# Optimization experiments

Hardware: AMD Instinct MI355X
Metric: run time of the kernel (lower is better)

Reference implementation:

```python
import jax, jax.numpy as jnp
import numpy as np

IN_CH = 256
OUT_CH = 256
NUM_HEADS = 4
LOCAL_RADIUS = 2
SCALE = OUT_CH ** 0.5  # torch divides by out_channels**0.5


def setup_inputs() -> dict:
    key = jax.random.key(0)
    ks = jax.random.split(key, 7)
    B, C, H, W = 1, IN_CH, 48, 48
    x = jax.random.normal(ks[0], (B, C, H, W), dtype=jnp.float32)
    s = 0.02
    Wq = jax.random.normal(ks[1], (OUT_CH, IN_CH), dtype=jnp.float32) * s
    Wk = jax.random.normal(ks[2], (OUT_CH, IN_CH), dtype=jnp.float32) * s
    Wv = jax.random.normal(ks[3], (OUT_CH, IN_CH), dtype=jnp.float32) * s
    bq = jax.random.normal(ks[4], (OUT_CH,), dtype=jnp.float32) * s
    bk = jax.random.normal(ks[5], (OUT_CH,), dtype=jnp.float32) * s
    bv = jax.random.normal(ks[6], (OUT_CH,), dtype=jnp.float32) * s
    return {"x": x, "Wq": Wq, "bq": bq, "Wk": Wk, "bk": bk, "Wv": Wv, "bv": bv}


def reference(x, Wq, bq, Wk, bk, Wv, bv):
    B, C, H, W = x.shape
    N = H * W
    # Faithful to torch: x.view(B, N, -1) is a raw reshape of [B,C,H,W]
    xr = x.reshape(B, N, C)
    q = xr @ Wq.T + bq  # [B, N, OUT_CH]
    k = xr @ Wk.T + bk
    v = xr @ Wv.T + bv
    dh = OUT_CH // NUM_HEADS
    # [B, heads, N, dh]
    q = q.reshape(B, N, NUM_HEADS, dh).transpose(0, 2, 1, 3)
    k = k.reshape(B, N, NUM_HEADS, dh).transpose(0, 2, 1, 3)
    v = v.reshape(B, N, NUM_HEADS, dh).transpose(0, 2, 1, 3)
    acc = jnp.zeros_like(v)
    for h in range(-LOCAL_RADIUS, LOCAL_RADIUS + 1):
        for w in range(-LOCAL_RADIUS, LOCAL_RADIUS + 1):
            # torch rolls dims (-3, -2) of [B, heads, N, dh] -> axes (1, 2)
            rk = jnp.roll(k, shift=(h, w), axis=(1, 2))
            scores = jnp.einsum('bhnd,bhmd->bhnm', q, rk) / SCALE
            p = jax.nn.softmax(scores, axis=-1)  # dropout p=0 -> identity
            rv = jnp.roll(v, shift=(-h, -w), axis=(1, 2))
            acc = acc + jnp.einsum('bhnm,bhmd->bhnd', p, rv)
    out = acc.transpose(0, 2, 1, 3).reshape(B, N, NUM_HEADS * dh)
    return out
```

## Files before the change

kernel.cpp:

```cpp
#include <hip/hip_runtime.h>


#define N_TOK 2304
#define OUTC 256
#define HSZ (N_TOK * 64)

typedef _Float16 half8 __attribute__((ext_vector_type(8)));
typedef _Float16 half4 __attribute__((ext_vector_type(4)));
typedef float f32x4 __attribute__((ext_vector_type(4)));

typedef __attribute__((address_space(3))) unsigned int as3_u32;
typedef __attribute__((address_space(1))) unsigned int as1_u32;

__device__ __forceinline__ f32x4 mfma16(half8 a, half8 b, f32x4 c) {
  return __builtin_amdgcn_mfma_f32_16x16x32_f16(a, b, c, 0, 0, 0);
}

__device__ __forceinline__ void gload_lds16(const _Float16* g, _Float16* l) {
  __builtin_amdgcn_global_load_lds((const as1_u32*)g, (as3_u32*)l, 16, 0, 0);
}

__global__ __launch_bounds__(256) void k_convert(
    const float* __restrict__ x, const float* __restrict__ Wq,
    const float* __restrict__ Wk, const float* __restrict__ Wv,
    _Float16* __restrict__ xh, _Float16* __restrict__ Wh) {
  int i = blockIdx.x * 256 + threadIdx.x;
  if (i < N_TOK * OUTC / 4) {
    float4 f = ((const float4*)x)[i];
    half4 h; h[0] = (_Float16)f.x; h[1] = (_Float16)f.y; h[2] = (_Float16)f.z; h[3] = (_Float16)f.w;
    ((half4*)xh)[i] = h;
  }
  if (i < OUTC * OUTC / 4) {
    float4 a = ((const float4*)Wq)[i];
    float4 b = ((const float4*)Wk)[i];
    float4 c = ((const float4*)Wv)[i];
    half4 ha, hb, hc;
    ha[0]=(_Float16)a.x; ha[1]=(_Float16)a.y; ha[2]=(_Float16)a.z; ha[3]=(_Float16)a.w;
    hb[0]=(_Float16)b.x; hb[1]=(_Float16)b.y; hb[2]=(_Float16)b.z; hb[3]=(_Float16)b.w;
    hc[0]=(_Float16)c.x; hc[1]=(_Float16)c.y; hc[2]=(_Float16)c.z; hc[3]=(_Float16)c.w;
    ((half4*)Wh)[i] = ha;
    ((half4*)(Wh + OUTC*OUTC))[i] = hb;
    ((half4*)(Wh + 2*OUTC*OUTC))[i] = hc;
  }
}

__global__ __launch_bounds__(256) void k_proj(
    const _Float16* __restrict__ xh, const _Float16* __restrict__ Wh,
    const float* __restrict__ bq, const float* __restrict__ bk,
    const float* __restrict__ bv,
    _Float16* __restrict__ Qh, _Float16* __restrict__ KF, float* __restrict__ VfT) {
  const int w = threadIdx.x >> 6, lane = threadIdx.x & 63;
  const int lr = lane & 15, lk = lane >> 4;
  const int n0 = blockIdx.x * 64 + w * 16;
  const int o0 = blockIdx.y * 64;
  const int mat = blockIdx.z;
  const _Float16* W = Wh + mat * (OUTC * OUTC);
  f32x4 acc[4] = {};
  const _Float16* xrow = xh + (n0 + lr) * OUTC + 8 * lk;
#pragma unroll
  for (int kk = 0; kk < 8; ++kk) {
    half8 a = *(const half8*)(xrow + 32 * kk);
#pragma unroll
    for (int c = 0; c < 4; ++c) {
      half8 b = *(const half8*)(W + (o0 + 16*c + lr) * OUTC + 32*kk + 8*lk);
      acc[c] = mfma16(a, b, acc[c]);
    }
  }
  const float* bias = (mat == 0) ? bq : (mat == 1) ? bk : bv;
  const int hd = blockIdx.y;
#pragma unroll
  for (int c = 0; c < 4; ++c) {
    int o = o0 + 16*c + lr;
    float bo = bias[o];
    if (mat == 2) {
      float4 vv;
      vv.x = acc[c][0] + bo; vv.y = acc[c][1] + bo;
      vv.z = acc[c][2] + bo; vv.w = acc[c][3] + bo;
      *(float4*)(VfT + (size_t)o * N_TOK + n0 + 4*lk) = vv;
    } else if (mat == 0) {
      int d = 16*c + lr;
      const float qs = 0.0625f * 1.4426950408889634f;
#pragma unroll
      for (int r = 0; r < 4; ++r) {
        int n = n0 + 4*lk + r;
        Qh[((size_t)hd * N_TOK + n) * 64 + d] = (_Float16)((acc[c][r] + bo) * qs);
      }
    } else {
      int d = 16*c + lr;
      int h = d >> 5, g4K = (d >> 3) & 3, iiK = d & 7;
#pragma unroll
      for (int r = 0; r < 4; ++r) {
        int n = n0 + 4*lk + r;
        int tK = n >> 6, cK = (n >> 4) & 3, lrK = n & 15;
        KF[(size_t)hd * HSZ + ((tK*4 + cK)*2 + h)*512 + (g4K*16 + lrK)*8 + iiK] =
            (_Float16)(acc[c][r] + bo);
      }
    }
  }
}

__global__ __launch_bounds__(256) void k_smooth(
    const float* __restrict__ VfT, _Float16* __restrict__ VF) {
  const int t = blockIdx.x, vh = blockIdx.y;
  for (int f = threadIdx.x; f < 512; f += 256) {
    int cc = f >> 7, h = (f >> 6) & 1, g4 = (f >> 4) & 3, lr = f & 15;
    const float* src = VfT + (size_t)(vh*64 + 16*cc + lr) * N_TOK;
    int jbase = t*64 + 32*h + 4*g4;
    half8 out;
#pragma unroll
    for (int i = 0; i < 8; ++i) {
      int j = jbase + 16*(i >> 2) + (i & 3);
      float s = 0.f;
#pragma unroll
      for (int w = -4; w <= 4; w += 2) s += src[(j + w + N_TOK) % N_TOK];
      out[i] = (_Float16)s;
    }
    *(half8*)(VF + (size_t)vh * HSZ + (size_t)t * 4096 + f * 8) = out;
  }
}

__global__ __launch_bounds__(256) void k_flash(
    const _Float16* __restrict__ Qh, const _Float16* __restrict__ KF,
    const _Float16* __restrict__ VF,
    _Float16* __restrict__ Opart, float* __restrict__ Lpart) {
  __shared__ __align__(16) _Float16 lds[2][8192];
  const int wv = threadIdx.x >> 6, lane = threadIdx.x & 63;
  const int lr = lane & 15, g4 = lane >> 4;
  const int strip = blockIdx.x * 4 + wv;
  const int n0 = strip * 16;
  const int pair = blockIdx.y;
  const int hd = pair >> 2, gk = pair & 3;
  const int chunk = blockIdx.z;
  const int vh = (2*hd + 4 - gk) & 3;

  const _Float16* Qp = Qh + ((size_t)hd * N_TOK + n0 + lr) * 64 + 8*g4;
  const half8 q0 = *(const half8*)(Qp);
  const half8 q1 = *(const half8*)(Qp + 32);

  const _Float16* Kt = KF + (size_t)gk * HSZ + (size_t)chunk * 9 * 4096;
  const _Float16* Vt = VF + (size_t)vh * HSZ + (size_t)chunk * 9 * 4096;
  const _Float16* gsrc = (wv < 2 ? Kt : Vt) + (wv & 1) * 2048 + lane * 8;
  const int ldsoff = (wv < 2 ? 0 : 4096) + (wv & 1) * 2048;

  f32x4 acc[4] = {};
  f32x4 accl = {};
  half8 ones;
#pragma unroll
  for (int i = 0; i < 8; ++i) ones[i] = (_Float16)1.0f;

  auto stage = [&](int t, int b) {
    const _Float16* s = gsrc + (size_t)t * 4096;
    _Float16* d = &lds[b][ldsoff];
    gload_lds16(s,        d);
    gload_lds16(s + 512,  d + 512);
    gload_lds16(s + 1024, d + 1024);
    gload_lds16(s + 1536, d + 1536);
  };
  auto body = [&](int b) {
    const _Float16* ldsK = &lds[b][0]    + lane * 8;
    const _Float16* ldsV = &lds[b][4096] + lane * 8;
    f32x4 s[4];
    __builtin_amdgcn_s_setprio(1);
#pragma unroll
    for (int c = 0; c < 4; ++c) {
      f32x4 t = {};
      t = mfma16(*(const half8*)(ldsK + c*1024),       q0, t);
      t = mfma16(*(const half8*)(ldsK + c*1024 + 512), q1, t);
      s[c] = t;
    }
    __builtin_amdgcn_s_setprio(0);
    float p[16];
#pragma unroll
    for (int c = 0; c < 4; ++c)
#pragma unroll
      for (int r = 0; r < 4; ++r) p[4*c + r] = exp2f(s[c][r]);
    half8 pb0, pb1;
#pragma unroll
    for (int ii = 0; ii < 8; ++ii) { pb0[ii] = (_Float16)p[ii]; pb1[ii] = (_Float16)p[8 + ii]; }
    __builtin_amdgcn_s_setprio(1);
#pragma unroll
    for (int cc = 0; cc < 4; ++cc) {
      acc[cc] = mfma16(*(const half8*)(ldsV + cc*1024),       pb0, acc[cc]);
      acc[cc] = mfma16(*(const half8*)(ldsV + cc*1024 + 512), pb1, acc[cc]);
    }
    accl = mfma16(ones, pb0, accl);
    accl = mfma16(ones, pb1, accl);
    __builtin_amdgcn_s_setprio(0);
  };

  stage(0, 0);
  __syncthreads();
#pragma unroll 1
  for (int t = 0; t < 9; ++t) {
    if (t < 8) stage(t + 1, (t + 1) & 1);
    body(t & 1);
    __syncthreads();
  }

  float inv = 1.0f / accl[0];
  _Float16* Od = Opart + (((size_t)chunk * 16 + pair) * N_TOK + n0 + lr) * 64;
#pragma unroll
  for (int cc = 0; cc < 4; ++cc) {
    half4 h;
#pragma unroll
    for (int r = 0; r < 4; ++r) h[r] = (_Float16)(acc[cc][r] * inv);
    *(half4*)(Od + 16*cc + 4*g4) = h;
  }
  if (g4 == 0)
    Lpart[((size_t)chunk * 16 + pair) * N_TOK + n0 + lr] = accl[0];
}

__global__ __launch_bounds__(256) void k_combine(
    const _Float16* __restrict__ Opart, const float* __restrict__ Lpart,
    float* __restrict__ out) {
  int gid = blockIdx.x * 256 + threadIdx.x;
  int hd = gid / (N_TOK * 8);
  int rem = gid % (N_TOK * 8);
  int n = rem >> 3, db = (rem & 7) * 8;
  float acc[8] = {};
#pragma unroll
  for (int gk = 0; gk < 4; ++gk) {
    float cg = (((hd - gk) & 3) == 2) ? 2.0f : 1.0f;
    int pair = hd * 4 + gk;
    float la[4], lsum = 0.f;
#pragma unroll
    for (int ch = 0; ch < 4; ++ch) {
      la[ch] = Lpart[((size_t)ch * 16 + pair) * N_TOK + n];
      lsum += la[ch];
    }
    float rs = cg / lsum;
#pragma unroll
    for (int ch = 0; ch < 4; ++ch) {
      half8 v = *(const half8*)(Opart + (((size_t)ch * 16 + pair) * N_TOK + n) * 64 + db);
      float w = la[ch] * rs;
#pragma unroll
      for (int i = 0; i < 8; ++i) acc[i] += w * (float)v[i];
    }
  }
  float* dst = out + (size_t)n * OUTC + hd * 64 + db;
  float4 r0, r1;
  r0.x = acc[0]; r0.y = acc[1]; r0.z = acc[2]; r0.w = acc[3];
  r1.x = acc[4]; r1.y = acc[5]; r1.z = acc[6]; r1.w = acc[7];
  *(float4*)(dst)     = r0;
  *(float4*)(dst + 4) = r1;
}

extern "C" void kernel_launch(void* const* d_in, const int* in_sizes, int n_in,
                              void* d_out, int out_size, void* d_ws, size_t ws_size,
                              hipStream_t stream) {
  (void)in_sizes; (void)n_in; (void)out_size; (void)ws_size;
  const float* x  = (const float*)d_in[0];
  const float* Wq = (const float*)d_in[1];
  const float* bq = (const float*)d_in[2];
  const float* Wk = (const float*)d_in[3];
  const float* bk = (const float*)d_in[4];
  const float* Wv = (const float*)d_in[5];
  const float* bv = (const float*)d_in[6];

  char* ws = (char*)d_ws;
  _Float16* xh  = (_Float16*)(ws);
  float*    Lp  = (float*)   (ws);
  _Float16* Wh  = (_Float16*)(ws + 1179648);
  _Float16* Qh  = (_Float16*)(ws + 1572864);
  _Float16* KF  = (_Float16*)(ws + 2752512);
  float*    VfT = (float*)   (ws + 3932160);
  _Float16* VF  = (_Float16*)(ws + 6291456);
  _Float16* Op  = (_Float16*)(ws + 7471104);
  float* out = (float*)d_out;

  k_convert<<<dim3(576), dim3(256), 0, stream>>>(x, Wq, Wk, Wv, xh, Wh);
  k_proj   <<<dim3(36, 4, 3), dim3(256), 0, stream>>>(xh, Wh, bq, bk, bv, Qh, KF, VfT);
  k_smooth <<<dim3(36, 4), dim3(256), 0, stream>>>(VfT, VF);
  k_flash  <<<dim3(36, 16, 4), dim3(256), 0, stream>>>(Qh, KF, VF, Op, Lp);
  k_combine<<<dim3(288), dim3(256), 0, stream>>>(Op, Lp, out);
}
```

Baseline: 73.97 us.

## Process two 16-row query strips per wave to reuse K/V tiles

Each wave now handles 32 query rows (two 16-row strips) instead of 16. It reuses every K and V fragment loaded from LDS for both strips, and the grid along x is halved. Each K/V chunk is therefore staged through LDS half as many times, which cuts global-to-LDS traffic and block overhead. The softmax exponent now uses the raw exp2 builtin with packed round-toward-zero fp16 conversion to trim ALU work. In exchange the kernel uses more registers and launches half as many blocks (1152 instead of 2304), which may lower occupancy and latency hiding.

```diff
diff --git a/kernel.cpp b/kernel.cpp
--- a/kernel.cpp
+++ b/kernel.cpp
@@ -7,6 +7,7 @@
 
 typedef _Float16 half8 __attribute__((ext_vector_type(8)));
 typedef _Float16 half4 __attribute__((ext_vector_type(4)));
+typedef __fp16 fp16x2 __attribute__((ext_vector_type(2)));
 typedef float f32x4 __attribute__((ext_vector_type(4)));
 
 typedef __attribute__((address_space(3))) unsigned int as3_u32;
@@ -19,6 +20,8 @@
 __device__ __forceinline__ void gload_lds16(const _Float16* g, _Float16* l) {
   __builtin_amdgcn_global_load_lds((const as1_u32*)g, (as3_u32*)l, 16, 0, 0);
 }
+
+union H8U { half8 h8; fp16x2 h2[4]; };
 
 __global__ __launch_bounds__(256) void k_convert(
     const float* __restrict__ x, const float* __restrict__ Wq,
@@ -127,23 +130,25 @@
   const int wv = threadIdx.x >> 6, lane = threadIdx.x & 63;
   const int lr = lane & 15, g4 = lane >> 4;
   const int strip = blockIdx.x * 4 + wv;
-  const int n0 = strip * 16;
+  const int n0 = strip * 32;
   const int pair = blockIdx.y;
   const int hd = pair >> 2, gk = pair & 3;
   const int chunk = blockIdx.z;
   const int vh = (2*hd + 4 - gk) & 3;
 
   const _Float16* Qp = Qh + ((size_t)hd * N_TOK + n0 + lr) * 64 + 8*g4;
-  const half8 q0 = *(const half8*)(Qp);
-  const half8 q1 = *(const half8*)(Qp + 32);
+  const half8 qa0 = *(const half8*)(Qp);
+  const half8 qa1 = *(const half8*)(Qp + 32);
+  const half8 qb0 = *(const half8*)(Qp + 16*64);
+  const half8 qb1 = *(const half8*)(Qp + 16*64 + 32);
 
   const _Float16* Kt = KF + (size_t)gk * HSZ + (size_t)chunk * 9 * 4096;
   const _Float16* Vt = VF + (size_t)vh * HSZ + (size_t)chunk * 9 * 4096;
   const _Float16* gsrc = (wv < 2 ? Kt : Vt) + (wv & 1) * 2048 + lane * 8;
   const int ldsoff = (wv < 2 ? 0 : 4096) + (wv & 1) * 2048;
 
-  f32x4 acc[4] = {};
-  f32x4 accl = {};
+  f32x4 accA[4] = {}, accB[4] = {};
+  f32x4 acclA = {}, acclB = {};
   half8 ones;
 #pragma unroll
   for (int i = 0; i < 8; ++i) ones[i] = (_Float16)1.0f;
@@ -159,32 +164,45 @@
   auto body = [&](int b) {
     const _Float16* ldsK = &lds[b][0]    + lane * 8;
     const _Float16* ldsV = &lds[b][4096] + lane * 8;
-    f32x4 s[4];
+    f32x4 sA[4], sB[4];
     __builtin_amdgcn_s_setprio(1);
 #pragma unroll
     for (int c = 0; c < 4; ++c) {
-      f32x4 t = {};
-      t = mfma16(*(const half8*)(ldsK + c*1024),       q0, t);
-      t = mfma16(*(const half8*)(ldsK + c*1024 + 512), q1, t);
-      s[c] = t;
+      half8 k0 = *(const half8*)(ldsK + c*1024);
+      half8 k1 = *(const half8*)(ldsK + c*1024 + 512);
+      f32x4 tA = {}; tA = mfma16(k0, qa0, tA); tA = mfma16(k1, qa1, tA); sA[c] = tA;
+      f32x4 tB = {}; tB = mfma16(k0, qb0, tB); tB = mfma16(k1, qb1, tB); sB[c] = tB;
     }
     __builtin_amdgcn_s_setprio(0);
-    float p[16];
-#pragma unroll
-    for (int c = 0; c < 4; ++c)
-#pragma unroll
-      for (int r = 0; r < 4; ++r) p[4*c + r] = exp2f(s[c][r]);
-    half8 pb0, pb1;
-#pragma unroll
-    for (int ii = 0; ii < 8; ++ii) { pb0[ii] = (_Float16)p[ii]; pb1[ii] = (_Float16)p[8 + ii]; }
+    H8U a0, a1, b0, b1;
+#pragma unroll
+    for (int c = 0; c < 4; ++c) {
+      float eA0 = __builtin_amdgcn_exp2f(sA[c][0]);
+      float eA1 = __builtin_amdgcn_exp2f(sA[c][1]);
+      float eA2 = __builtin_amdgcn_exp2f(sA[c][2]);
+      float eA3 = __builtin_amdgcn_exp2f(sA[c][3]);
+      float eB0 = __builtin_amdgcn_exp2f(sB[c][0]);
+      float eB1 = __builtin_amdgcn_exp2f(sB[c][1]);
+      float eB2 = __builtin_amdgcn_exp2f(sB[c][2]);
+      float eB3 = __builtin_amdgcn_exp2f(sB[c][3]);
+      H8U* da = (c < 2) ? &a0 : &a1;
+      H8U* db = (c < 2) ? &b0 : &b1;
+      int base = (c & 1) * 2;
+      da->h2[base]     = __builtin_amdgcn_cvt_pkrtz(eA0, eA1);
+      da->h2[base + 1] = __builtin_amdgcn_cvt_pkrtz(eA2, eA3);
+      db->h2[base]     = __builtin_amdgcn_cvt_pkrtz(eB0, eB1);
+      db->h2[base + 1] = __builtin_amdgcn_cvt_pkrtz(eB2, eB3);
+    }
     __builtin_amdgcn_s_setprio(1);
 #pragma unroll
     for (int cc = 0; cc < 4; ++cc) {
-      acc[cc] = mfma16(*(const half8*)(ldsV + cc*1024),       pb0, acc[cc]);
-      acc[cc] = mfma16(*(const half8*)(ldsV + cc*1024 + 512), pb1, acc[cc]);
-    }
-    accl = mfma16(ones, pb0, accl);
-    accl = mfma16(ones, pb1, accl);
+      half8 v0 = *(const half8*)(ldsV + cc*1024);
+      half8 v1 = *(const half8*)(ldsV + cc*1024 + 512);
+      accA[cc] = mfma16(v0, a0.h8, accA[cc]); accA[cc] = mfma16(v1, a1.h8, accA[cc]);
+      accB[cc] = mfma16(v0, b0.h8, accB[cc]); accB[cc] = mfma16(v1, b1.h8, accB[cc]);
+    }
+    acclA = mfma16(ones, a0.h8, acclA); acclA = mfma16(ones, a1.h8, acclA);
+    acclB = mfma16(ones, b0.h8, acclB); acclB = mfma16(ones, b1.h8, acclB);
     __builtin_amdgcn_s_setprio(0);
   };
 
@@ -197,17 +215,25 @@
     __syncthreads();
   }
 
-  float inv = 1.0f / accl[0];
-  _Float16* Od = Opart + (((size_t)chunk * 16 + pair) * N_TOK + n0 + lr) * 64;
+  float invA = 1.0f / acclA[0];
+  float invB = 1.0f / acclB[0];
+  _Float16* Oa = Opart + (((size_t)chunk * 16 + pair) * N_TOK + n0 + lr) * 64;
+  _Float16* Ob = Oa + 16 * 64;
 #pragma unroll
   for (int cc = 0; cc < 4; ++cc) {
-    half4 h;
-#pragma unroll
-    for (int r = 0; r < 4; ++r) h[r] = (_Float16)(acc[cc][r] * inv);
-    *(half4*)(Od + 16*cc + 4*g4) = h;
-  }
-  if (g4 == 0)
-    Lpart[((size_t)chunk * 16 + pair) * N_TOK + n0 + lr] = accl[0];
+    half4 ha, hb;
+#pragma unroll
+    for (int r = 0; r < 4; ++r) {
+      ha[r] = (_Float16)(accA[cc][r] * invA);
+      hb[r] = (_Float16)(accB[cc][r] * invB);
+    }
+    *(half4*)(Oa + 16*cc + 4*g4) = ha;
+    *(half4*)(Ob + 16*cc + 4*g4) = hb;
+  }
+  if (g4 == 0) {
+    Lpart[((size_t)chunk * 16 + pair) * N_TOK + n0 + lr] = acclA[0];
+    Lpart[((size_t)chunk * 16 + pair) * N_TOK + n0 + 16 + lr] = acclB[0];
+  }
 }
 
 __global__ __launch_bounds__(256) void k_combine(
@@ -271,6 +297,6 @@
   k_convert<<<dim3(576), dim3(256), 0, stream>>>(x, Wq, Wk, Wv, xh, Wh);
   k_proj   <<<dim3(36, 4, 3), dim3(256), 0, stream>>>(xh, Wh, bq, bk, bv, Qh, KF, VfT);
   k_smooth <<<dim3(36, 4), dim3(256), 0, stream>>>(VfT, VF);
-  k_flash  <<<dim3(36, 16, 4), dim3(256), 0, stream>>>(Qh, KF, VF, Op, Lp);
+  k_flash  <<<dim3(18, 16, 4), dim3(256), 0, stream>>>(Qh, KF, VF, Op, Lp);
   k_combine<<<dim3(288), dim3(256), 0, stream>>>(Op, Lp, out);
 }
```

Result: faster. 67.46 us (-8.8%).
